# Kernel tuning notes

Hardware: AMD Instinct MI355X
Metric: run time of the kernel (lower is better)

## Reference

```python
import jax, jax.numpy as jnp
import numpy as np

EPS = 0.0001
N_NODES = 8192
N_GRAPHS = 128
NODES_PER_G = 64
N_FEAT = 128
CLDIM = 512
LAYERS = 3
HEADS = 8
HID = 64
N_EDGES = 262144
N_CLASSES = 10


def setup_inputs():
    key = jax.random.key(0)
    ks = jax.random.split(key, 12)
    x = jax.random.normal(ks[0], (N_NODES, N_FEAT), jnp.float32)

    def rand_edges(k):
        k1, k2 = jax.random.split(k)
        g = jax.random.randint(k1, (N_EDGES,), 0, N_GRAPHS)
        loc = jax.random.randint(k2, (2, N_EDGES), 0, NODES_PER_G)
        return (g[None, :] * NODES_PER_G + loc).astype(jnp.int32)

    edge_index = rand_edges(ks[1])
    neg_edge_index = rand_edges(ks[2])
    batch = (jnp.arange(N_NODES) // NODES_PER_G).astype(jnp.int32)
    # mask indices: all within-graph node pairs (block-diagonal mask==1)
    base = jnp.arange(N_GRAPHS) * NODES_PER_G
    a = jnp.repeat(jnp.arange(NODES_PER_G), NODES_PER_G)
    b = jnp.tile(jnp.arange(NODES_PER_G), NODES_PER_G)
    midx = jnp.stack([
        (base[:, None] + a[None, :]).reshape(-1),
        (base[:, None] + b[None, :]).reshape(-1),
    ]).astype(jnp.int32)
    s = 0.05
    return dict(
        x=x, edge_index=edge_index, neg_edge_index=neg_edge_index,
        batch=batch, midx=midx,
        fc_W=jax.random.normal(ks[3], (N_FEAT, CLDIM), jnp.float32) * s,
        fc_b=jnp.zeros((CLDIM,), jnp.float32),
        bn_g=jnp.ones((LAYERS, CLDIM), jnp.float32),
        bn_b=jnp.zeros((LAYERS, CLDIM), jnp.float32),
        conv_W=jax.random.normal(ks[4], (LAYERS, CLDIM, CLDIM), jnp.float32) * s,
        conv_b=jnp.zeros((LAYERS, CLDIM), jnp.float32),
        feat_W=jax.random.normal(ks[5], (LAYERS * CLDIM, HEADS * HID), jnp.float32) * s,
        phi=jax.random.normal(ks[6], (HEADS, 2 * HID, 1), jnp.float32) * s,
        fc1_W=jax.random.normal(ks[7], (HEADS * HID, HID), jnp.float32) * s,
        fc1_b=jnp.zeros((HID,), jnp.float32),
        fc2_W=jax.random.normal(ks[8], (HID, N_CLASSES), jnp.float32) * s,
        fc2_b=jnp.zeros((N_CLASSES,), jnp.float32),
    )


def _bn(h, g, b):
    # BatchNorm1d in training mode (biased variance over nodes)
    m = jnp.mean(h, 0)
    v = jnp.var(h, 0)
    return (h - m) * jax.lax.rsqrt(v + 1e-5) * g + b


def _gcn(h, W, b, src, dst, n):
    # GCNConv with added self-loops: D^-1/2 (A+I) D^-1/2 (h W) + b
    h2 = h @ W
    deg = jax.ops.segment_sum(jnp.ones(src.shape[0], h.dtype), dst, n) + 1.0
    dinv = jax.lax.rsqrt(deg)
    coef = (dinv[src] * dinv[dst])[:, None]
    agg = jax.ops.segment_sum(h2[src] * coef, dst, n)
    return agg + h2 / deg[:, None] + b


def _forward(x, fc_W, fc_b, bn_g, bn_b, conv_W, conv_b, feat_W, phi,
             fc1_W, fc1_b, fc2_W, fc2_b, edge_index, neg_edge_index, batch, midx):
    n = x.shape[0]
    h = x @ fc_W + fc_b
    src, dst = edge_index[0], edge_index[1]
    hs = []
    for i in range(LAYERS):
        h = _bn(h, bn_g[i], bn_b[i])
        h = jax.nn.relu(_gcn(h, conv_W[i], conv_b[i], src, dst, n))
        hs.append(h)
    z = jnp.concatenate(hs, -1)  # [N, LAYERS*CLDIM]

    # ---- recon loss: per-edge inner-product decoder, mean-pooled per graph ----
    def edge_loss(ei, neg):
        v = jnp.sum(z[ei[0]] * z[ei[1]], -1)
        sgm = jax.nn.sigmoid(v)
        l = -jnp.log(EPS + (1.0 - sgm if neg else sgm))
        seg = batch[ei[0]]
        cnt = jax.ops.segment_sum(jnp.ones_like(l), seg, N_GRAPHS)
        tot = jax.ops.segment_sum(l, seg, N_GRAPHS)
        return jnp.sum(tot / jnp.maximum(cnt, 1.0))

    Lrc = (edge_loss(edge_index, False) + edge_loss(neg_edge_index, True)) / N_GRAPHS

    # ---- classifier: multi-head sigmoid attention over mask pairs ----
    xh = (z @ feat_W).reshape(n, HEADS, HID)
    phi_a = phi[:, :HID, 0]   # [H, HID]
    phi_b = phi[:, HID:, 0]   # [H, HID]
    # cat([x_i, x_j]) @ phi == x_i @ phi_a + x_j @ phi_b, computed per node then gathered
    s1 = jnp.einsum('nhd,hd->nh', xh, phi_a)
    s2 = jnp.einsum('nhd,hd->nh', xh, phi_b)
    w = jax.nn.sigmoid(jax.nn.leaky_relu(s1[midx[0]] + s2[midx[1]]))  # [M, H]
    msg = (xh[midx[1]] * w[:, :, None]).reshape(-1, HEADS * HID)      # [M, H*HID]
    agg = jax.ops.segment_sum(msg, midx[0], n)
    logits = jax.nn.leaky_relu(agg @ fc1_W + fc1_b) @ fc2_W + fc2_b
    tmp = jnp.exp(logits - jnp.max(logits, -1, keepdims=True)) + EPS
    preds = tmp / jnp.sum(tmp, -1, keepdims=True)
    cnt = jax.ops.segment_sum(jnp.ones((n,), preds.dtype), batch, N_GRAPHS)
    yp = jax.ops.segment_sum(preds, batch, N_GRAPHS) / cnt[:, None]
    return jnp.log(yp), Lrc, preds


def reference(x, edge_index, neg_edge_index, batch, midx, fc_W, fc_b, bn_g, bn_b,
              conv_W, conv_b, feat_W, phi, fc1_W, fc1_b, fc2_W, fc2_b):
    return _forward(x, fc_W, fc_b, bn_g, bn_b, conv_W, conv_b, feat_W, phi,
                    fc1_W, fc1_b, fc2_W, fc2_b, edge_index, neg_edge_index, batch, midx)
```

## Files before the change

kernel.cpp:

```cpp
#include <hip/hip_runtime.h>

#define NN 8192
#define NG 128
#define NF 128
#define CL 512
#define ZD 1536
#define NE 262144

typedef __attribute__((ext_vector_type(8))) _Float16 half8;
typedef __attribute__((ext_vector_type(4))) float f32x4;

__global__ void deg_kernel(const int* __restrict__ dst, float* __restrict__ deg) {
    int e = blockIdx.x * 256 + threadIdx.x;
    atomicAdd(&deg[dst[e]], 1.0f);
}

__global__ void deg_finish(float* __restrict__ deg, float* __restrict__ dinv) {
    int n = blockIdx.x * 256 + threadIdx.x;
    float d = deg[n] + 1.0f;
    deg[n] = d;
    dinv[n] = rsqrtf(d);
}

__global__ void build_adj(const int* __restrict__ src, const int* __restrict__ dst,
                          const float* __restrict__ dinv, float* __restrict__ A) {
    int e = blockIdx.x * 256 + threadIdx.x;
    int s = src[e], d = dst[e];
    int g = d >> 6;
    atomicAdd(&A[(size_t)((g << 6) + (d & 63)) * 64 + (s & 63)], dinv[s] * dinv[d]);
}

__global__ void adj_diag(const float* __restrict__ deg, float* __restrict__ A) {
    int n = blockIdx.x * 256 + threadIdx.x;
    int g = n >> 6, i = n & 63;
    A[(size_t)(g * 64 + i) * 64 + i] += 1.0f / deg[n];
}

__global__ void cvtA(const float* __restrict__ Amat, _Float16* __restrict__ Ah) {
    int t = blockIdx.x * 256 + threadIdx.x;
    int i4 = t * 4;
    int g = i4 >> 12, loc = i4 & 4095;
    float4 v = *(const float4*)(Amat + (size_t)g * 4096 + loc);
    float vv[4] = {v.x, v.y, v.z, v.w};
    int row = loc >> 6;
    int swz = (row & 7) << 3;
    #pragma unroll
    for (int e = 0; e < 4; ++e)
        Ah[(size_t)g * 4096 + ((loc + e) ^ swz)] = (_Float16)vv[e];
}

__global__ void cvt_h(const float* __restrict__ in, _Float16* __restrict__ out) {
    int i = blockIdx.x * 256 + threadIdx.x;
    float4 a = *(const float4*)(in + (size_t)i * 8);
    float4 b = *(const float4*)(in + (size_t)i * 8 + 4);
    half8 o;
    o[0] = (_Float16)a.x; o[1] = (_Float16)a.y; o[2] = (_Float16)a.z; o[3] = (_Float16)a.w;
    o[4] = (_Float16)b.x; o[5] = (_Float16)b.y; o[6] = (_Float16)b.z; o[7] = (_Float16)b.w;
    *(half8*)(out + (size_t)i * 8) = o;
}

__global__ void cvtT(const float* __restrict__ W, _Float16* __restrict__ Wt,
                     int Kd, int Nd) {
    __shared__ float t[32][33];
    int kb = blockIdx.y * 32, nb = blockIdx.x * 32;
    int tx = threadIdx.x, ty = threadIdx.y;
    for (int i = ty; i < 32; i += 8)
        t[i][tx] = W[(size_t)(kb + i) * Nd + nb + tx];
    __syncthreads();
    for (int i = ty; i < 32; i += 8)
        Wt[(size_t)(nb + i) * Kd + kb + tx] = (_Float16)t[tx][i];
}

__global__ void wprep(const float* __restrict__ W,
                      const float* __restrict__ sums, const float* __restrict__ sqs,
                      const float* __restrict__ g, const float* __restrict__ b,
                      _Float16* __restrict__ Wt, float* __restrict__ bias2,
                      int Kd, int Nd) {
    __shared__ float t[32][33];
    __shared__ float tks[32];
    int kb = blockIdx.y * 32, nb = blockIdx.x * 32;
    int tx = threadIdx.x, ty = threadIdx.y;
    for (int i = ty; i < 32; i += 8)
        t[i][tx] = W[(size_t)(kb + i) * Nd + nb + tx];
    int kc = kb + tx;
    float m = sums[kc] * (1.0f / NN);
    float var = sqs[kc] * (1.0f / NN) - m * m;
    float sc = rsqrtf(var + 1e-5f) * g[kc];
    if (ty == 0) tks[tx] = b[kc] - m * sc;
    __syncthreads();
    for (int i = ty; i < 32; i += 8)
        Wt[(size_t)(nb + i) * Kd + kb + tx] = (_Float16)(t[tx][i] * sc);
    if (ty == 0) {
        float acc = 0.f;
        #pragma unroll
        for (int i = 0; i < 32; ++i) acc = fmaf(tks[i], t[i][tx], acc);
        atomicAdd(&bias2[nb + tx], acc);
    }
}

template<int ACT, bool HASB, bool OUT16, bool STATS, bool FUSE>
__global__ __launch_bounds__(256)
void gemm_f16(const _Float16* __restrict__ A, int lda,
              const _Float16* __restrict__ Bt, int ldb,
              float* __restrict__ Cf, _Float16* __restrict__ Ch, int ldc,
              const float* __restrict__ bias, int K,
              float* __restrict__ sums, float* __restrict__ sqs,
              const _Float16* __restrict__ Ahg,
              const float* __restrict__ cb,
              _Float16* __restrict__ Zout)
{
    __shared__ __align__(16) char SMraw[FUSE ? 34816 : 24576];
    _Float16* As = (_Float16*)SMraw;
    _Float16* Bs = (_Float16*)(SMraw + 16384);
    const int tid = threadIdx.x;
    const int lane = tid & 63, wave = tid >> 6;
    const int wr = wave >> 1, wc = wave & 1;
    const int ntile = gridDim.x;
    const int li = blockIdx.y * ntile + blockIdx.x;
    const int x8 = li & 7, rest = li >> 3;
    const int bt = rest % ntile;
    const int bp = (rest / ntile) * 8 + x8;
    const int bm = bp * 128, bn = bt * 64;

    f32x4 acc[4][2];
    #pragma unroll
    for (int m = 0; m < 4; ++m)
        #pragma unroll
        for (int n = 0; n < 2; ++n)
            acc[m][n] = (f32x4){0.f, 0.f, 0.f, 0.f};

    const int fl = lane & 15, kh = (lane >> 4) * 8;
    const int sw = (fl & 7) << 3;

    for (int k0 = 0; k0 < K; k0 += 64) {
        #pragma unroll
        for (int j = 0; j < 4; ++j) {
            int d = wave * 2048 + j * 512 + lane * 8;
            int row = d >> 6, kk = d & 63;
            int sk = kk ^ ((row & 7) << 3);
            __builtin_amdgcn_global_load_lds(
                (const __attribute__((address_space(1))) void*)(A + (size_t)(bm + row) * lda + k0 + sk),
                (__attribute__((address_space(3))) void*)&As[wave * 2048 + j * 512], 16, 0, 0);
        }
        #pragma unroll
        for (int j = 0; j < 2; ++j) {
            int d = wave * 1024 + j * 512 + lane * 8;
            int row = d >> 6, kk = d & 63;
            int sk = kk ^ ((row & 7) << 3);
            __builtin_amdgcn_global_load_lds(
                (const __attribute__((address_space(1))) void*)(Bt + (size_t)(bn + row) * ldb + k0 + sk),
                (__attribute__((address_space(3))) void*)&Bs[wave * 1024 + j * 512], 16, 0, 0);
        }
        __syncthreads();
        #pragma unroll
        for (int kc = 0; kc < 2; ++kc) {
            int ko = (kc * 32 + kh) ^ sw;
            half8 av[4], bv[2];
            #pragma unroll
            for (int m = 0; m < 4; ++m)
                av[m] = *(const half8*)&As[(wr * 64 + m * 16 + fl) * 64 + ko];
            #pragma unroll
            for (int n = 0; n < 2; ++n)
                bv[n] = *(const half8*)&Bs[(wc * 32 + n * 16 + fl) * 64 + ko];
            #pragma unroll
            for (int m = 0; m < 4; ++m)
                #pragma unroll
                for (int n = 0; n < 2; ++n)
                    acc[m][n] = __builtin_amdgcn_mfma_f32_16x16x32_f16(av[m], bv[n], acc[m][n], 0, 0, 0);
        }
        __syncthreads();
    }

    const int orow0 = (lane >> 4) * 4;
    const int ocol  = lane & 15;

    if constexpr (!FUSE) {
        #pragma unroll
        for (int n = 0; n < 2; ++n) {
            int col = bn + wc * 32 + n * 16 + ocol;
            float bb = HASB ? bias[col] : 0.f;
            float ss = 0.f, qq = 0.f;
            #pragma unroll
            for (int m = 0; m < 4; ++m) {
                #pragma unroll
                for (int r = 0; r < 4; ++r) {
                    int rowg = bm + wr * 64 + m * 16 + orow0 + r;
                    float v = acc[m][n][r] + bb;
                    if (ACT == 2) v = v > 0.f ? v : 0.01f * v;
                    if (STATS) { ss += v; qq = fmaf(v, v, qq); }
                    if (OUT16) Ch[(size_t)rowg * ldc + col] = (_Float16)v;
                    else       Cf[(size_t)rowg * ldc + col] = v;
                }
            }
            if (STATS) {
                ss += __shfl_down(ss, 32); ss += __shfl_down(ss, 16);
                qq += __shfl_down(qq, 32); qq += __shfl_down(qq, 16);
                if (lane < 16) {
                    atomicAdd(&sums[col], ss);
                    atomicAdd(&sqs[col], qq);
                }
            }
        }
    } else {
        _Float16* AsA = (_Float16*)SMraw;
        _Float16* Xs  = (_Float16*)(SMraw + 16384);
        const _Float16* Ag = Ahg + (size_t)(bm >> 6) * 4096;
        #pragma unroll
        for (int j = 0; j < 4; ++j)
            __builtin_amdgcn_global_load_lds(
                (const __attribute__((address_space(1))) void*)(Ag + wave * 2048 + j * 512 + lane * 8),
                (__attribute__((address_space(3))) void*)&AsA[wave * 2048 + j * 512], 16, 0, 0);
        #pragma unroll
        for (int n = 0; n < 2; ++n) {
            int c = wc * 32 + n * 16 + ocol;
            float bb = HASB ? bias[bn + c] : 0.f;
            int csw = (c & 7) << 3;
            #pragma unroll
            for (int m = 0; m < 4; ++m) {
                #pragma unroll
                for (int r = 0; r < 4; ++r) {
                    int srow = wr * 64 + m * 16 + orow0 + r;
                    Xs[c * 128 + (srow & 64) + ((srow & 63) ^ csw)] = (_Float16)(acc[m][n][r] + bb);
                }
            }
        }
        __syncthreads();
        const int gg = wave >> 1, rh = wave & 1;
        f32x4 acc2[2][4];
        #pragma unroll
        for (int m2 = 0; m2 < 2; ++m2)
            #pragma unroll
            for (int n2 = 0; n2 < 4; ++n2)
                acc2[m2][n2] = (f32x4){0.f, 0.f, 0.f, 0.f};
        #pragma unroll
        for (int kc = 0; kc < 2; ++kc) {
            int ko = (kc * 32 + kh) ^ sw;
            #pragma unroll
            for (int m2 = 0; m2 < 2; ++m2) {
                int arow = rh * 32 + m2 * 16 + fl;
                half8 av = *(const half8*)&AsA[gg * 4096 + arow * 64 + ko];
                #pragma unroll
                for (int n2 = 0; n2 < 4; ++n2) {
                    int c = n2 * 16 + fl;
                    half8 bv = *(const half8*)&Xs[c * 128 + gg * 64 + ((kc * 32 + kh) ^ ((c & 7) << 3))];
                    acc2[m2][n2] = __builtin_amdgcn_mfma_f32_16x16x32_f16(av, bv, acc2[m2][n2], 0, 0, 0);
                }
            }
        }
        __syncthreads();
        float* Cs = (float*)SMraw;
        #pragma unroll
        for (int m2 = 0; m2 < 2; ++m2)
            #pragma unroll
            for (int n2 = 0; n2 < 4; ++n2)
                #pragma unroll
                for (int r = 0; r < 4; ++r)
                    Cs[(gg * 64 + rh * 32 + m2 * 16 + orow0 + r) * 68 + n2 * 16 + ocol] = acc2[m2][n2][r];
        __syncthreads();
        const int rr = tid >> 3, dq = tid & 7;
        #pragma unroll
        for (int pass = 0; pass < 4; ++pass) {
            int row = pass * 32 + rr;
            half8 hv;
            #pragma unroll
            for (int e = 0; e < 8; ++e) {
                float v = Cs[row * 68 + dq * 8 + e] + cb[bn + dq * 8 + e];
                v = v > 0.f ? v : 0.f;
                hv[e] = (_Float16)v;
            }
            *(half8*)(Zout + (size_t)(bm + row) * ZD + bn + dq * 8) = hv;
        }
        if (STATS && tid < 64) {
            float bb = cb[bn + tid];
            float ss = 0.f, qq = 0.f;
            for (int row = 0; row < 128; ++row) {
                float v = Cs[row * 68 + tid] + bb;
                v = v > 0.f ? v : 0.f;
                ss += v;
                qq = fmaf(v, v, qq);
            }
            atomicAdd(&sums[bn + tid], ss);
            atomicAdd(&sqs[bn + tid], qq);
        }
    }
}

__global__ __launch_bounds__(256)
void gram_mfma(const _Float16* __restrict__ Z, float* __restrict__ G)
{
    __shared__ _Float16 Zs[4096];
    const int g = blockIdx.x;
    const int tid = threadIdx.x;
    const int lane = tid & 63, wave = tid >> 6;
    const int fl = lane & 15, kh = (lane >> 4) * 8;
    const int sw = (fl & 7) << 3;

    f32x4 acc[4];
    #pragma unroll
    for (int n = 0; n < 4; ++n) acc[n] = (f32x4){0.f, 0.f, 0.f, 0.f};

    for (int k0 = 0; k0 < ZD; k0 += 64) {
        #pragma unroll
        for (int j = 0; j < 2; ++j) {
            int d = wave * 1024 + j * 512 + lane * 8;
            int row = d >> 6, kk = d & 63;
            int sk = kk ^ ((row & 7) << 3);
            __builtin_amdgcn_global_load_lds(
                (const __attribute__((address_space(1))) void*)(Z + (size_t)(g * 64 + row) * ZD + k0 + sk),
                (__attribute__((address_space(3))) void*)&Zs[wave * 1024 + j * 512], 16, 0, 0);
        }
        __syncthreads();
        #pragma unroll
        for (int kc = 0; kc < 2; ++kc) {
            int ko = (kc * 32 + kh) ^ sw;
            half8 av = *(const half8*)&Zs[(wave * 16 + fl) * 64 + ko];
            #pragma unroll
            for (int n = 0; n < 4; ++n) {
                half8 bv = *(const half8*)&Zs[(n * 16 + fl) * 64 + ko];
                acc[n] = __builtin_amdgcn_mfma_f32_16x16x32_f16(av, bv, acc[n], 0, 0, 0);
            }
        }
        __syncthreads();
    }
    const int orow0 = (lane >> 4) * 4;
    const int ocol  = lane & 15;
    #pragma unroll
    for (int n = 0; n < 4; ++n)
        #pragma unroll
        for (int r = 0; r < 4; ++r)
            G[(size_t)(g * 64 + wave * 16 + orow0 + r) * 64 + n * 16 + ocol] = acc[n][r];
}

__global__ void edge_loss2(const int* __restrict__ ei, const int* __restrict__ nei,
                           const float* __restrict__ G, float* __restrict__ LOSS)
{
    const int setid = blockIdx.y;
    const int* e0 = setid ? nei : ei;
    const int* e1 = e0 + NE;
    float* tot = LOSS + setid * 256;
    float* cnt = tot + 128;
    __shared__ float lt[128];
    __shared__ float lc[128];
    int tid = threadIdx.x;
    if (tid < 128) { lt[tid] = 0.f; lc[tid] = 0.f; }
    __syncthreads();
    for (int e = blockIdx.x * blockDim.x + tid; e < NE; e += gridDim.x * blockDim.x) {
        int a = e0[e], b = e1[e];
        int g = a >> 6;
        float v = G[(size_t)((g << 6) + (a & 63)) * 64 + (b & 63)];
        float s = 1.f / (1.f + expf(-v));
        float p = setid ? (1.f - s) : s;
        float l = -logf(1e-4f + p);
        atomicAdd(&lt[g], l);
        atomicAdd(&lc[g], 1.f);
    }
    __syncthreads();
    if (tid < 128) {
        atomicAdd(&tot[tid], lt[tid]);
        atomicAdd(&cnt[tid], lc[tid]);
    }
}

__global__ void lrc_final(const float* __restrict__ loss, float* __restrict__ out)
{
    int t = threadIdx.x;
    float v = loss[t] / fmaxf(loss[128 + t], 1.f) + loss[256 + t] / fmaxf(loss[384 + t], 1.f);
    __shared__ float red[128];
    red[t] = v;
    __syncthreads();
    for (int s = 64; s; s >>= 1) {
        if (t < s) red[t] += red[t + s];
        __syncthreads();
    }
    if (t == 0) out[0] = red[0] * (1.0f / 128.0f);
}

__global__ __launch_bounds__(256)
void attn_fused(const _Float16* __restrict__ xh, const float* __restrict__ phi,
                _Float16* __restrict__ agg)
{
    const int g = blockIdx.x, h = blockIdx.y;
    __shared__ _Float16 Xt[4096];
    __shared__ _Float16 Ws[4096];
    __shared__ float Cs[64 * 68];
    __shared__ float s1s[64], s2s[64];
    const int tid = threadIdx.x;
    {
        const int b = tid >> 2, dq = tid & 3;
        const _Float16* xr = xh + (size_t)(g * 64 + b) * CL + h * 64 + dq * 16;
        const float* pa = phi + h * 128 + dq * 16;
        const float* pb = pa + 64;
        float sa = 0.f, sb = 0.f;
        #pragma unroll
        for (int j = 0; j < 2; ++j) {
            half8 v = *(const half8*)(xr + j * 8);
            float4 A4 = *(const float4*)(pa + j * 8);
            float4 A5 = *(const float4*)(pa + j * 8 + 4);
            float4 B4 = *(const float4*)(pb + j * 8);
            float4 B5 = *(const float4*)(pb + j * 8 + 4);
            float aa[8] = {A4.x, A4.y, A4.z, A4.w, A5.x, A5.y, A5.z, A5.w};
            float bb[8] = {B4.x, B4.y, B4.z, B4.w, B5.x, B5.y, B5.z, B5.w};
            #pragma unroll
            for (int e = 0; e < 8; ++e) {
                int d = dq * 16 + j * 8 + e;
                float vf = (float)v[e];
                Xt[(d * 64 + b) ^ ((d & 7) << 3)] = v[e];
                sa = fmaf(vf, aa[e], sa);
                sb = fmaf(vf, bb[e], sb);
            }
        }
        sa += __shfl_down(sa, 2); sa += __shfl_down(sa, 1);
        sb += __shfl_down(sb, 2); sb += __shfl_down(sb, 1);
        if (dq == 0) { s1s[b] = sa; s2s[b] = sb; }
    }
    __syncthreads();
    {
        const int i = tid >> 2, bq = tid & 3;
        float si = s1s[i];
        #pragma unroll
        for (int e = 0; e < 16; ++e) {
            int b = bq * 16 + e;
            float t = si + s2s[b];
            t = t > 0.f ? t : 0.01f * t;
            float w = 1.f / (1.f + expf(-t));
            Ws[(i * 64 + b) ^ ((i & 7) << 3)] = (_Float16)w;
        }
    }
    __syncthreads();
    const int lane = tid & 63, wave = tid >> 6;
    const int fl = lane & 15, kh = (lane >> 4) * 8;
    f32x4 acc[4];
    #pragma unroll
    for (int n = 0; n < 4; ++n) acc[n] = (f32x4){0.f, 0.f, 0.f, 0.f};
    #pragma unroll
    for (int kc = 0; kc < 2; ++kc) {
        int rowa = wave * 16 + fl;
        half8 av = *(const half8*)&Ws[(rowa * 64 + kc * 32 + kh) ^ ((rowa & 7) << 3)];
        #pragma unroll
        for (int n = 0; n < 4; ++n) {
            int rowb = n * 16 + fl;
            half8 bv = *(const half8*)&Xt[(rowb * 64 + kc * 32 + kh) ^ ((rowb & 7) << 3)];
            acc[n] = __builtin_amdgcn_mfma_f32_16x16x32_f16(av, bv, acc[n], 0, 0, 0);
        }
    }
    const int orow0 = (lane >> 4) * 4, ocol = lane & 15;
    #pragma unroll
    for (int n = 0; n < 4; ++n)
        #pragma unroll
        for (int r = 0; r < 4; ++r)
            Cs[(wave * 16 + orow0 + r) * 68 + n * 16 + ocol] = acc[n][r];
    __syncthreads();
    {
        const int rr = tid >> 3, dq = tid & 7;
        #pragma unroll
        for (int half = 0; half < 2; ++half) {
            int nd = half * 32 + rr;
            half8 hv;
            #pragma unroll
            for (int e = 0; e < 8; ++e)
                hv[e] = (_Float16)Cs[nd * 68 + dq * 8 + e];
            *(half8*)(agg + (size_t)(g * 64 + nd) * CL + h * 64 + dq * 8) = hv;
        }
    }
}

__global__ void head_yp(const float* __restrict__ hid, const float* __restrict__ fc2W,
                        const float* __restrict__ fc2b,
                        float* __restrict__ preds, float* __restrict__ outlog)
{
    int g = blockIdx.x, lane = threadIdx.x;
    int n = g * 64 + lane;
    const float* hr = hid + (size_t)n * 64;
    float x[64];
    #pragma unroll
    for (int k = 0; k < 64; ++k) x[k] = hr[k];
    float lg[10];
    float mx = -1e30f;
    #pragma unroll
    for (int c = 0; c < 10; ++c) {
        float s = fc2b[c];
        #pragma unroll
        for (int k = 0; k < 64; ++k) s = fmaf(x[k], fc2W[k * 10 + c], s);
        lg[c] = s;
        mx = fmaxf(mx, s);
    }
    float sum = 0.f;
    #pragma unroll
    for (int c = 0; c < 10; ++c) {
        float t = expf(lg[c] - mx) + 1e-4f;
        lg[c] = t;
        sum += t;
    }
    float inv = 1.f / sum;
    #pragma unroll
    for (int c = 0; c < 10; ++c) {
        lg[c] *= inv;
        preds[(size_t)n * 10 + c] = lg[c];
    }
    #pragma unroll
    for (int off = 32; off; off >>= 1)
        #pragma unroll
        for (int c = 0; c < 10; ++c) lg[c] += __shfl_down(lg[c], off);
    if (lane == 0)
        #pragma unroll
        for (int c = 0; c < 10; ++c) outlog[g * 10 + c] = logf(lg[c] * (1.0f / 64.0f));
}

extern "C" void kernel_launch(void* const* d_in, const int* in_sizes, int n_in,
                              void* d_out, int out_size, void* d_ws, size_t ws_size,
                              hipStream_t stream)
{
    (void)in_sizes; (void)n_in; (void)out_size; (void)ws_size;
    const float* x     = (const float*)d_in[0];
    const int*   ei    = (const int*)d_in[1];
    const int*   nei   = (const int*)d_in[2];
    const float* fcW   = (const float*)d_in[5];
    const float* fcb   = (const float*)d_in[6];
    const float* bng   = (const float*)d_in[7];
    const float* bnb   = (const float*)d_in[8];
    const float* convW = (const float*)d_in[9];
    const float* convb = (const float*)d_in[10];
    const float* featW = (const float*)d_in[11];
    const float* phi   = (const float*)d_in[12];
    const float* fc1W  = (const float*)d_in[13];
    const float* fc1b  = (const float*)d_in[14];
    const float* fc2W  = (const float*)d_in[15];
    const float* fc2b  = (const float*)d_in[16];
    float* out = (float*)d_out;

    char* ws = (char*)d_ws;
    _Float16* Z       = (_Float16*)(ws);
    _Float16* H0      = (_Float16*)(ws + 25165824);
    _Float16* AGG     = (_Float16*)(ws + 33554432);
    _Float16* xb      = (_Float16*)(ws + 41943040);
    _Float16* fcWt    = (_Float16*)(ws + 44040192);
    _Float16* convWs  = (_Float16*)(ws + 44171264);
    _Float16* featWt  = (_Float16*)(ws + 44695552);
    _Float16* fc1Wt   = (_Float16*)(ws + 46268416);
    _Float16* Ah      = (_Float16*)(ws + 46333952);
    float*    Gram    = (float*)(ws + 47382528);
    float*    DINV    = (float*)(ws + 49479680);
    float*    HID     = (float*)(ws + 49512448);
    float*    DEG     = (float*)(ws + 51609600);
    float*    Amat    = (float*)(ws + 51642368);
    float*    LOSS    = (float*)(ws + 53739520);
    float*    BNS3    = (float*)(ws + 53741568);
    float*    B2      = (float*)(ws + 53753856);
    _Float16* XH      = H0;

    const int* src = ei;
    const int* dst = ei + NE;

    hipMemsetAsync(DEG, 0, 53760000 - 51609600, stream);

    deg_kernel<<<NE / 256, 256, 0, stream>>>(dst, DEG);
    deg_finish<<<NN / 256, 256, 0, stream>>>(DEG, DINV);
    build_adj<<<NE / 256, 256, 0, stream>>>(src, dst, DINV, Amat);
    adj_diag<<<NN / 256, 256, 0, stream>>>(DEG, Amat);
    cvtA<<<(NG * 4096 / 4) / 256, 256, 0, stream>>>(Amat, Ah);

    cvt_h<<<(NN * NF / 8) / 256, 256, 0, stream>>>(x, xb);
    cvtT<<<dim3(CL / 32, NF / 32), dim3(32, 8), 0, stream>>>(fcW, fcWt, NF, CL);
    cvtT<<<dim3(CL / 32, ZD / 32), dim3(32, 8), 0, stream>>>(featW, featWt, ZD, CL);
    cvtT<<<dim3(2, 16), dim3(32, 8), 0, stream>>>(fc1W, fc1Wt, 512, 64);

    gemm_f16<0, true, true, true, false><<<dim3(CL / 64, NN / 128), 256, 0, stream>>>(
        xb, NF, fcWt, NF, nullptr, H0, CL, fcb, NF, BNS3, BNS3 + 512,
        nullptr, nullptr, nullptr);

    for (int i = 0; i < 3; ++i) {
        const _Float16* Ain = (i == 0) ? H0 : (Z + (size_t)(i - 1) * CL);
        int lda = (i == 0) ? CL : ZD;
        float* sums = BNS3 + i * 1024;
        float* sqs  = sums + 512;
        float* b2   = B2 + i * 512;
        wprep<<<dim3(CL / 32, CL / 32), dim3(32, 8), 0, stream>>>(
            convW + (size_t)i * CL * CL, sums, sqs, bng + i * CL, bnb + i * CL,
            convWs, b2, CL, CL);
        if (i < 2)
            gemm_f16<0, true, false, true, true><<<dim3(CL / 64, NN / 128), 256, 0, stream>>>(
                Ain, lda, convWs, CL, nullptr, nullptr, 0, b2, CL,
                BNS3 + (i + 1) * 1024, BNS3 + (i + 1) * 1024 + 512,
                Ah, convb + i * CL, Z + (size_t)i * CL);
        else
            gemm_f16<0, true, false, false, true><<<dim3(CL / 64, NN / 128), 256, 0, stream>>>(
                Ain, lda, convWs, CL, nullptr, nullptr, 0, b2, CL,
                nullptr, nullptr, Ah, convb + i * CL, Z + (size_t)i * CL);
    }

    gram_mfma<<<NG, 256, 0, stream>>>(Z, Gram);
    edge_loss2<<<dim3(128, 2), 256, 0, stream>>>(ei, nei, Gram, LOSS);
    lrc_final<<<1, 128, 0, stream>>>(LOSS, out + 1280);

    gemm_f16<0, false, true, false, false><<<dim3(CL / 64, NN / 128), 256, 0, stream>>>(
        Z, ZD, featWt, ZD, nullptr, XH, CL, nullptr, ZD, nullptr, nullptr,
        nullptr, nullptr, nullptr);

    attn_fused<<<dim3(NG, 8), 256, 0, stream>>>(XH, phi, AGG);

    gemm_f16<2, true, false, false, false><<<dim3(1, NN / 128), 256, 0, stream>>>(
        AGG, CL, fc1Wt, CL, HID, nullptr, 64, fc1b, CL, nullptr, nullptr,
        nullptr, nullptr, nullptr);

    head_yp<<<NG, 64, 0, stream>>>(HID, fc2W, fc2b, out + 1281, out);
}
```

Before: 196.5 us.

## Fuse feature GEMM into attention, fc1 into head, merge adjacency prep kernels

Folds the degree finish and diagonal-add kernels into build_adj and cvtA, computing rsqrt of degree on the fly. Splits the per-graph Gram GEMM over two K halves for more blocks, and edge_loss sums the two partial Gram matrices. Fuses the feature projection GEMM into the per-graph, per-head attention kernel, and fuses the fc1 GEMM with the fc2/softmax head. The aim is fewer launches and no intermediate XH/HID round trips through global memory, at the cost of less parallelism in the fused kernels and an extra Gram buffer read in edge_loss.

```diff
diff --git a/kernel.cpp b/kernel.cpp
--- a/kernel.cpp
+++ b/kernel.cpp
@@ -15,34 +15,26 @@
     atomicAdd(&deg[dst[e]], 1.0f);
 }
 
-__global__ void deg_finish(float* __restrict__ deg, float* __restrict__ dinv) {
-    int n = blockIdx.x * 256 + threadIdx.x;
-    float d = deg[n] + 1.0f;
-    deg[n] = d;
-    dinv[n] = rsqrtf(d);
-}
-
 __global__ void build_adj(const int* __restrict__ src, const int* __restrict__ dst,
-                          const float* __restrict__ dinv, float* __restrict__ A) {
+                          const float* __restrict__ deg, float* __restrict__ A) {
     int e = blockIdx.x * 256 + threadIdx.x;
     int s = src[e], d = dst[e];
     int g = d >> 6;
-    atomicAdd(&A[(size_t)((g << 6) + (d & 63)) * 64 + (s & 63)], dinv[s] * dinv[d]);
-}
-
-__global__ void adj_diag(const float* __restrict__ deg, float* __restrict__ A) {
-    int n = blockIdx.x * 256 + threadIdx.x;
-    int g = n >> 6, i = n & 63;
-    A[(size_t)(g * 64 + i) * 64 + i] += 1.0f / deg[n];
-}
-
-__global__ void cvtA(const float* __restrict__ Amat, _Float16* __restrict__ Ah) {
+    float w = rsqrtf(deg[s] + 1.0f) * rsqrtf(deg[d] + 1.0f);
+    atomicAdd(&A[(size_t)((g << 6) + (d & 63)) * 64 + (s & 63)], w);
+}
+
+__global__ void cvtA(const float* __restrict__ Amat, const float* __restrict__ deg,
+                     _Float16* __restrict__ Ah) {
     int t = blockIdx.x * 256 + threadIdx.x;
     int i4 = t * 4;
     int g = i4 >> 12, loc = i4 & 4095;
     float4 v = *(const float4*)(Amat + (size_t)g * 4096 + loc);
     float vv[4] = {v.x, v.y, v.z, v.w};
     int row = loc >> 6;
+    int c0 = loc & 63;
+    int ed = row - c0;
+    if (ed >= 0 && ed < 4) vv[ed] += 1.0f / (deg[g * 64 + row] + 1.0f);
     int swz = (row & 7) << 3;
     #pragma unroll
     for (int e = 0; e < 4; ++e)
@@ -286,20 +278,21 @@
 }
 
 __global__ __launch_bounds__(256)
-void gram_mfma(const _Float16* __restrict__ Z, float* __restrict__ G)
+void gram_mfma(const _Float16* __restrict__ Z, float* __restrict__ Gparts)
 {
     __shared__ _Float16 Zs[4096];
-    const int g = blockIdx.x;
+    const int g = blockIdx.x, khalf = blockIdx.y;
     const int tid = threadIdx.x;
     const int lane = tid & 63, wave = tid >> 6;
     const int fl = lane & 15, kh = (lane >> 4) * 8;
     const int sw = (fl & 7) << 3;
+    float* G = Gparts + (size_t)khalf * NG * 4096;
 
     f32x4 acc[4];
     #pragma unroll
     for (int n = 0; n < 4; ++n) acc[n] = (f32x4){0.f, 0.f, 0.f, 0.f};
 
-    for (int k0 = 0; k0 < ZD; k0 += 64) {
+    for (int k0 = khalf * (ZD / 2); k0 < (khalf + 1) * (ZD / 2); k0 += 64) {
         #pragma unroll
         for (int j = 0; j < 2; ++j) {
             int d = wave * 1024 + j * 512 + lane * 8;
@@ -332,13 +325,14 @@
 }
 
 __global__ void edge_loss2(const int* __restrict__ ei, const int* __restrict__ nei,
-                           const float* __restrict__ G, float* __restrict__ LOSS)
+                           const float* __restrict__ G0, float* __restrict__ LOSS)
 {
     const int setid = blockIdx.y;
     const int* e0 = setid ? nei : ei;
     const int* e1 = e0 + NE;
     float* tot = LOSS + setid * 256;
     float* cnt = tot + 128;
+    const float* G1 = G0 + (size_t)NG * 4096;
     __shared__ float lt[128];
     __shared__ float lc[128];
     int tid = threadIdx.x;
@@ -347,7 +341,8 @@
     for (int e = blockIdx.x * blockDim.x + tid; e < NE; e += gridDim.x * blockDim.x) {
         int a = e0[e], b = e1[e];
         int g = a >> 6;
-        float v = G[(size_t)((g << 6) + (a & 63)) * 64 + (b & 63)];
+        size_t idx = (size_t)((g << 6) + (a & 63)) * 64 + (b & 63);
+        float v = G0[idx] + G1[idx];
         float s = 1.f / (1.f + expf(-v));
         float p = setid ? (1.f - s) : s;
         float l = -logf(1e-4f + p);
@@ -376,38 +371,72 @@
 }
 
 __global__ __launch_bounds__(256)
-void attn_fused(const _Float16* __restrict__ xh, const float* __restrict__ phi,
-                _Float16* __restrict__ agg)
+void featattn(const _Float16* __restrict__ Z, const _Float16* __restrict__ featWt,
+              const float* __restrict__ phi, _Float16* __restrict__ agg)
 {
-    const int g = blockIdx.x, h = blockIdx.y;
-    __shared__ _Float16 Xt[4096];
-    __shared__ _Float16 Ws[4096];
-    __shared__ float Cs[64 * 68];
-    __shared__ float s1s[64], s2s[64];
+    __shared__ __align__(16) char SMraw[34816];
+    _Float16* As = (_Float16*)SMraw;
+    _Float16* Bs = (_Float16*)(SMraw + 8192);
+    float*    Cs = (float*)SMraw;
+    _Float16* Xt = (_Float16*)(SMraw + 17408);
+    _Float16* Ws = (_Float16*)(SMraw + 25600);
+    float*    s1s = (float*)(SMraw + 33792);
+    float*    s2s = (float*)(SMraw + 34048);
+    const int h = blockIdx.x, g = blockIdx.y;
     const int tid = threadIdx.x;
+    const int lane = tid & 63, wave = tid >> 6;
+    const int fl = lane & 15, kh = (lane >> 4) * 8;
+    const int sw = (fl & 7) << 3;
+
+    f32x4 acc[4];
+    #pragma unroll
+    for (int n = 0; n < 4; ++n) acc[n] = (f32x4){0.f, 0.f, 0.f, 0.f};
+
+    for (int k0 = 0; k0 < ZD; k0 += 64) {
+        #pragma unroll
+        for (int j = 0; j < 2; ++j) {
+            int d = wave * 1024 + j * 512 + lane * 8;
+            int row = d >> 6, kk = d & 63;
+            int sk = kk ^ ((row & 7) << 3);
+            __builtin_amdgcn_global_load_lds(
+                (const __attribute__((address_space(1))) void*)(Z + (size_t)(g * 64 + row) * ZD + k0 + sk),
+                (__attribute__((address_space(3))) void*)&As[wave * 1024 + j * 512], 16, 0, 0);
+            __builtin_amdgcn_global_load_lds(
+                (const __attribute__((address_space(1))) void*)(featWt + (size_t)(h * 64 + row) * ZD + k0 + sk),
+                (__attribute__((address_space(3))) void*)&Bs[wave * 1024 + j * 512], 16, 0, 0);
+        }
+        __syncthreads();
+        #pragma unroll
+        for (int kc = 0; kc < 2; ++kc) {
+            int ko = (kc * 32 + kh) ^ sw;
+            half8 av = *(const half8*)&As[(wave * 16 + fl) * 64 + ko];
+            #pragma unroll
+            for (int n = 0; n < 4; ++n) {
+                half8 bv = *(const half8*)&Bs[(n * 16 + fl) * 64 + ko];
+                acc[n] = __builtin_amdgcn_mfma_f32_16x16x32_f16(av, bv, acc[n], 0, 0, 0);
+            }
+        }
+        __syncthreads();
+    }
+    const int orow0 = (lane >> 4) * 4, ocol = lane & 15;
+    #pragma unroll
+    for (int n = 0; n < 4; ++n)
+        #pragma unroll
+        for (int r = 0; r < 4; ++r)
+            Cs[(wave * 16 + orow0 + r) * 68 + n * 16 + ocol] = acc[n][r];
+    __syncthreads();
     {
         const int b = tid >> 2, dq = tid & 3;
-        const _Float16* xr = xh + (size_t)(g * 64 + b) * CL + h * 64 + dq * 16;
         const float* pa = phi + h * 128 + dq * 16;
         const float* pb = pa + 64;
         float sa = 0.f, sb = 0.f;
         #pragma unroll
-        for (int j = 0; j < 2; ++j) {
-            half8 v = *(const half8*)(xr + j * 8);
-            float4 A4 = *(const float4*)(pa + j * 8);
-            float4 A5 = *(const float4*)(pa + j * 8 + 4);
-            float4 B4 = *(const float4*)(pb + j * 8);
-            float4 B5 = *(const float4*)(pb + j * 8 + 4);
-            float aa[8] = {A4.x, A4.y, A4.z, A4.w, A5.x, A5.y, A5.z, A5.w};
-            float bb[8] = {B4.x, B4.y, B4.z, B4.w, B5.x, B5.y, B5.z, B5.w};
-            #pragma unroll
-            for (int e = 0; e < 8; ++e) {
-                int d = dq * 16 + j * 8 + e;
-                float vf = (float)v[e];
-                Xt[(d * 64 + b) ^ ((d & 7) << 3)] = v[e];
-                sa = fmaf(vf, aa[e], sa);
-                sb = fmaf(vf, bb[e], sb);
-            }
+        for (int j = 0; j < 16; ++j) {
+            int d = dq * 16 + j;
+            float vf = Cs[b * 68 + d];
+            Xt[(d * 64 + b) ^ ((d & 7) << 3)] = (_Float16)vf;
+            sa = fmaf(vf, pa[j], sa);
+            sb = fmaf(vf, pb[j], sb);
         }
         sa += __shfl_down(sa, 2); sa += __shfl_down(sa, 1);
         sb += __shfl_down(sb, 2); sb += __shfl_down(sb, 1);
@@ -427,11 +456,9 @@
         }
     }
     __syncthreads();
-    const int lane = tid & 63, wave = tid >> 6;
-    const int fl = lane & 15, kh = (lane >> 4) * 8;
-    f32x4 acc[4];
-    #pragma unroll
-    for (int n = 0; n < 4; ++n) acc[n] = (f32x4){0.f, 0.f, 0.f, 0.f};
+    f32x4 acc2[4];
+    #pragma unroll
+    for (int n = 0; n < 4; ++n) acc2[n] = (f32x4){0.f, 0.f, 0.f, 0.f};
     #pragma unroll
     for (int kc = 0; kc < 2; ++kc) {
         int rowa = wave * 16 + fl;
@@ -440,15 +467,15 @@
         for (int n = 0; n < 4; ++n) {
             int rowb = n * 16 + fl;
             half8 bv = *(const half8*)&Xt[(rowb * 64 + kc * 32 + kh) ^ ((rowb & 7) << 3)];
-            acc[n] = __builtin_amdgcn_mfma_f32_16x16x32_f16(av, bv, acc[n], 0, 0, 0);
-        }
-    }
-    const int orow0 = (lane >> 4) * 4, ocol = lane & 15;
+            acc2[n] = __builtin_amdgcn_mfma_f32_16x16x32_f16(av, bv, acc2[n], 0, 0, 0);
+        }
+    }
+    __syncthreads();
     #pragma unroll
     for (int n = 0; n < 4; ++n)
         #pragma unroll
         for (int r = 0; r < 4; ++r)
-            Cs[(wave * 16 + orow0 + r) * 68 + n * 16 + ocol] = acc[n][r];
+            Cs[(wave * 16 + orow0 + r) * 68 + n * 16 + ocol] = acc2[n][r];
     __syncthreads();
     {
         const int rr = tid >> 3, dq = tid & 7;
@@ -464,46 +491,97 @@
     }
 }
 
-__global__ void head_yp(const float* __restrict__ hid, const float* __restrict__ fc2W,
-                        const float* __restrict__ fc2b,
-                        float* __restrict__ preds, float* __restrict__ outlog)
+__global__ __launch_bounds__(256)
+void fc1head(const _Float16* __restrict__ AGG, const _Float16* __restrict__ fc1Wt,
+             const float* __restrict__ fc1b,
+             const float* __restrict__ fc2W, const float* __restrict__ fc2b,
+             float* __restrict__ preds, float* __restrict__ outlog)
 {
-    int g = blockIdx.x, lane = threadIdx.x;
-    int n = g * 64 + lane;
-    const float* hr = hid + (size_t)n * 64;
-    float x[64];
-    #pragma unroll
-    for (int k = 0; k < 64; ++k) x[k] = hr[k];
-    float lg[10];
-    float mx = -1e30f;
-    #pragma unroll
-    for (int c = 0; c < 10; ++c) {
-        float s = fc2b[c];
-        #pragma unroll
-        for (int k = 0; k < 64; ++k) s = fmaf(x[k], fc2W[k * 10 + c], s);
-        lg[c] = s;
-        mx = fmaxf(mx, s);
-    }
-    float sum = 0.f;
-    #pragma unroll
-    for (int c = 0; c < 10; ++c) {
-        float t = expf(lg[c] - mx) + 1e-4f;
-        lg[c] = t;
-        sum += t;
-    }
-    float inv = 1.f / sum;
-    #pragma unroll
-    for (int c = 0; c < 10; ++c) {
-        lg[c] *= inv;
-        preds[(size_t)n * 10 + c] = lg[c];
-    }
-    #pragma unroll
-    for (int off = 32; off; off >>= 1)
-        #pragma unroll
-        for (int c = 0; c < 10; ++c) lg[c] += __shfl_down(lg[c], off);
-    if (lane == 0)
-        #pragma unroll
-        for (int c = 0; c < 10; ++c) outlog[g * 10 + c] = logf(lg[c] * (1.0f / 64.0f));
+    __shared__ __align__(16) char SMraw[17664];
+    _Float16* As = (_Float16*)SMraw;
+    _Float16* Bs = (_Float16*)(SMraw + 8192);
+    float*    Cs = (float*)SMraw;
+    const int g = blockIdx.x;
+    const int tid = threadIdx.x;
+    const int lane = tid & 63, wave = tid >> 6;
+    const int fl = lane & 15, kh = (lane >> 4) * 8;
+    const int sw = (fl & 7) << 3;
+
+    f32x4 acc[4];
+    #pragma unroll
+    for (int n = 0; n < 4; ++n) acc[n] = (f32x4){0.f, 0.f, 0.f, 0.f};
+
+    for (int k0 = 0; k0 < CL; k0 += 64) {
+        #pragma unroll
+        for (int j = 0; j < 2; ++j) {
+            int d = wave * 1024 + j * 512 + lane * 8;
+            int row = d >> 6, kk = d & 63;
+            int sk = kk ^ ((row & 7) << 3);
+            __builtin_amdgcn_global_load_lds(
+                (const __attribute__((address_space(1))) void*)(AGG + (size_t)(g * 64 + row) * CL + k0 + sk),
+                (__attribute__((address_space(3))) void*)&As[wave * 1024 + j * 512], 16, 0, 0);
+            __builtin_amdgcn_global_load_lds(
+                (const __attribute__((address_space(1))) void*)(fc1Wt + (size_t)row * CL + k0 + sk),
+                (__attribute__((address_space(3))) void*)&Bs[wave * 1024 + j * 512], 16, 0, 0);
+        }
+        __syncthreads();
+        #pragma unroll
+        for (int kc = 0; kc < 2; ++kc) {
+            int ko = (kc * 32 + kh) ^ sw;
+            half8 av = *(const half8*)&As[(wave * 16 + fl) * 64 + ko];
+            #pragma unroll
+            for (int n = 0; n < 4; ++n) {
+                half8 bv = *(const half8*)&Bs[(n * 16 + fl) * 64 + ko];
+                acc[n] = __builtin_amdgcn_mfma_f32_16x16x32_f16(av, bv, acc[n], 0, 0, 0);
+            }
+        }
+        __syncthreads();
+    }
+    const int orow0 = (lane >> 4) * 4, ocol = lane & 15;
+    #pragma unroll
+    for (int n = 0; n < 4; ++n) {
+        int col = n * 16 + ocol;
+        float bb = fc1b[col];
+        #pragma unroll
+        for (int r = 0; r < 4; ++r) {
+            float v = acc[n][r] + bb;
+            v = v > 0.f ? v : 0.01f * v;
+            Cs[(wave * 16 + orow0 + r) * 69 + col] = v;
+        }
+    }
+    __syncthreads();
+    if (tid < 64) {
+        float lg[10];
+        float mx = -1e30f;
+        #pragma unroll
+        for (int c = 0; c < 10; ++c) {
+            float s = fc2b[c];
+            #pragma unroll
+            for (int k = 0; k < 64; ++k) s = fmaf(Cs[tid * 69 + k], fc2W[k * 10 + c], s);
+            lg[c] = s;
+            mx = fmaxf(mx, s);
+        }
+        float sum = 0.f;
+        #pragma unroll
+        for (int c = 0; c < 10; ++c) {
+            float t = expf(lg[c] - mx) + 1e-4f;
+            lg[c] = t;
+            sum += t;
+        }
+        float inv = 1.f / sum;
+        #pragma unroll
+        for (int c = 0; c < 10; ++c) {
+            lg[c] *= inv;
+            preds[(size_t)(g * 64 + tid) * 10 + c] = lg[c];
+        }
+        #pragma unroll
+        for (int off = 32; off; off >>= 1)
+            #pragma unroll
+            for (int c = 0; c < 10; ++c) lg[c] += __shfl_down(lg[c], off);
+        if (tid == 0)
+            #pragma unroll
+            for (int c = 0; c < 10; ++c) outlog[g * 10 + c] = logf(lg[c] * (1.0f / 64.0f));
+    }
 }
 
 extern "C" void kernel_launch(void* const* d_in, const int* in_sizes, int n_in,
@@ -539,25 +617,20 @@
     _Float16* fc1Wt   = (_Float16*)(ws + 46268416);
     _Float16* Ah      = (_Float16*)(ws + 46333952);
     float*    Gram    = (float*)(ws + 47382528);
-    float*    DINV    = (float*)(ws + 49479680);
-    float*    HID     = (float*)(ws + 49512448);
-    float*    DEG     = (float*)(ws + 51609600);
-    float*    Amat    = (float*)(ws + 51642368);
-    float*    LOSS    = (float*)(ws + 53739520);
-    float*    BNS3    = (float*)(ws + 53741568);
-    float*    B2      = (float*)(ws + 53753856);
-    _Float16* XH      = H0;
+    float*    DEG     = (float*)(ws + 51576832);
+    float*    Amat    = (float*)(ws + 51609600);
+    float*    LOSS    = (float*)(ws + 53706752);
+    float*    BNS3    = (float*)(ws + 53708800);
+    float*    B2      = (float*)(ws + 53721088);
 
     const int* src = ei;
     const int* dst = ei + NE;
 
-    hipMemsetAsync(DEG, 0, 53760000 - 51609600, stream);
+    hipMemsetAsync(DEG, 0, 53727232 - 51576832, stream);
 
     deg_kernel<<<NE / 256, 256, 0, stream>>>(dst, DEG);
-    deg_finish<<<NN / 256, 256, 0, stream>>>(DEG, DINV);
-    build_adj<<<NE / 256, 256, 0, stream>>>(src, dst, DINV, Amat);
-    adj_diag<<<NN / 256, 256, 0, stream>>>(DEG, Amat);
-    cvtA<<<(NG * 4096 / 4) / 256, 256, 0, stream>>>(Amat, Ah);
+    build_adj<<<NE / 256, 256, 0, stream>>>(src, dst, DEG, Amat);
+    cvtA<<<(NG * 4096 / 4) / 256, 256, 0, stream>>>(Amat, DEG, Ah);
 
     cvt_h<<<(NN * NF / 8) / 256, 256, 0, stream>>>(x, xb);
     cvtT<<<dim3(CL / 32, NF / 32), dim3(32, 8), 0, stream>>>(fcW, fcWt, NF, CL);
@@ -588,19 +661,11 @@
                 nullptr, nullptr, Ah, convb + i * CL, Z + (size_t)i * CL);
     }
 
-    gram_mfma<<<NG, 256, 0, stream>>>(Z, Gram);
+    gram_mfma<<<dim3(NG, 2), 256, 0, stream>>>(Z, Gram);
     edge_loss2<<<dim3(128, 2), 256, 0, stream>>>(ei, nei, Gram, LOSS);
     lrc_final<<<1, 128, 0, stream>>>(LOSS, out + 1280);
 
-    gemm_f16<0, false, true, false, false><<<dim3(CL / 64, NN / 128), 256, 0, stream>>>(
-        Z, ZD, featWt, ZD, nullptr, XH, CL, nullptr, ZD, nullptr, nullptr,
-        nullptr, nullptr, nullptr);
-
-    attn_fused<<<dim3(NG, 8), 256, 0, stream>>>(XH, phi, AGG);
-
-    gemm_f16<2, true, false, false, false><<<dim3(1, NN / 128), 256, 0, stream>>>(
-        AGG, CL, fc1Wt, CL, HID, nullptr, 64, fc1b, CL, nullptr, nullptr,
-        nullptr, nullptr, nullptr);
-
-    head_yp<<<NG, 64, 0, stream>>>(HID, fc2W, fc2b, out + 1281, out);
-}
+    featattn<<<dim3(8, NG), 256, 0, stream>>>(Z, featWt, phi, AGG);
+
+    fc1head<<<NG, 256, 0, stream>>>(AGG, fc1Wt, fc1b, fc2W, fc2b, out + 1281, out);
+}
```

Result: faster. 187.6 us (-4.5%).
